# Optimization experiments

Hardware: AMD Instinct MI355X
Metric: run time of the kernel (lower is better)

## Reference

```python
import jax, jax.numpy as jnp
import numpy as np

N_NODES = 10000
N_EDGES = 160000
N_HEADS = 2
N_IN = 16   # fc input dim = x channels (15) + 1 dist channel
N_OUT = 32
ALPHA = 0.2
B, T_LEN = 2, 8


def setup_inputs() -> dict:
    key = jax.random.key(0)
    ks = jax.random.split(key, 6)
    x = jax.random.normal(ks[0], (B, T_LEN, N_NODES, N_IN - 1), dtype=jnp.float32)
    d_ew = jax.random.uniform(ks[1], (N_EDGES + N_NODES, N_HEADS), dtype=jnp.float32)
    u_edges = jax.random.randint(ks[2], (N_EDGES, 2), 0, N_NODES, dtype=jnp.int64)
    u_dist = jax.random.uniform(ks[3], (N_EDGES,), dtype=jnp.float32)
    W = jax.random.normal(ks[4], (N_OUT, N_IN), dtype=jnp.float32) * (1.0 / np.sqrt(N_IN))
    b = jax.random.normal(ks[5], (N_OUT,), dtype=jnp.float32) * 0.01
    return {"x": x, "T": T_LEN, "d_ew": d_ew, "u_edges": u_edges,
            "u_dist": u_dist, "W": W, "b": b}


def reference(x, T, d_ew, u_edges, u_dist, W, b):
    # d_edges = [u_edges; self-loops], d_dist = [u_dist; zeros]
    loops = jnp.arange(N_NODES, dtype=u_edges.dtype)
    d_edges = jnp.concatenate([u_edges, jnp.stack([loops, loops], axis=1)], axis=0)
    d_dist = jnp.concatenate([u_dist, jnp.zeros((N_NODES,), dtype=u_dist.dtype)], axis=0)
    node_i, node_j = d_edges[:, 0], d_edges[:, 1]

    Bx, t, _, C = x.shape
    # graph convolution: out[:, :, j] = sum_e{j(e)=j} d_ew[e] * x[:, :, i(e)]
    xg = x[:, :, node_i, :]                               # (B, t, E, C)
    msgs = xg[..., None, :] * d_ew[None, None, :, :, None]  # (B, t, E, H, C)
    x_conv = jnp.zeros((Bx, t, N_NODES, N_HEADS, C), dtype=x.dtype)
    x_conv = x_conv.at[:, :, node_j].add(msgs)            # (B, t, N, H, C)

    # dist convolution: (N, H)
    dist_conv = jnp.zeros((N_NODES, N_HEADS), dtype=d_ew.dtype)
    dist_conv = dist_conv.at[node_j].add(d_dist[:, None] * d_ew)

    # concat dist channel, broadcast over (B, t)
    dist_b = jnp.broadcast_to(dist_conv[None, None, :, :, None],
                              (Bx, t, N_NODES, N_HEADS, 1))
    x_feature = jnp.concatenate([x_conv, dist_b], axis=-1)  # (B, t, N, H, C+1)

    x_out = jnp.einsum('btnhc,oc->btnho', x_feature, W) + b

    # temporal alpha-blend (RHS uses pre-update values, as in torch slice assign)
    x_out = jnp.concatenate(
        [x_out[:, :1], ALPHA * x_out[:, :-1] + (1.0 - ALPHA) * x_out[:, 1:]], axis=1)
    return jax.nn.sigmoid(x_out)
```

## Files before the change

### kernel.cpp

```cpp
#include <hip/hip_runtime.h>
#include <hip/hip_bf16.h>

#define NN 10000
#define NE 160000
#define NBT 16
#define CIN 15
#define HPAD 128
#define BCAP 64
#define NOUT 32
#define ALPHA_F 0.2f

#define TRANS_BLKS 625
#define EDGE_BLKS  625

__device__ __forceinline__ float bf2f(unsigned short u) {
    return __uint_as_float(((unsigned int)u) << 16);
}
__device__ __forceinline__ unsigned short f2bf(float f) {
    __hip_bfloat16 h = __float2bfloat16(f);
    return *(unsigned short*)&h;
}

__global__ __launch_bounds__(256) void zero_ws(int* __restrict__ p) {
    int i = blockIdx.x * 256 + threadIdx.x;
    if (i < NN) p[i] = 0;
}

__global__ __launch_bounds__(256) void prep(const float* __restrict__ x,
                                            const int* __restrict__ edges,
                                            const float* __restrict__ dist,
                                            const float* __restrict__ dew,
                                            unsigned short* __restrict__ xh,
                                            int* __restrict__ cursor,
                                            int2* __restrict__ epay) {
    __shared__ float tile[NBT][16 * CIN];
    int bid = blockIdx.x;
    int tid = threadIdx.x;
    if (bid < TRANS_BLKS) {
        int n0 = bid * 16;
        if (tid < 16 * CIN) {
#pragma unroll
            for (int bt = 0; bt < NBT; ++bt)
                tile[bt][tid] = x[((size_t)bt * NN + n0) * CIN + tid];
        }
        __syncthreads();
        for (int g = tid; g < 16 * 2 * HPAD; g += 256) {
            int ln = g >> 8;
            int r  = g & 255;
            int half = r >> 7;
            int rr = r & 127;
            float v = 0.f;
            if (rr < 120) {
                int bt = half * 8 + rr / CIN;
                int c  = rr % CIN;
                v = tile[bt][ln * CIN + c];
            }
            xh[(size_t)(n0 + ln) * 256 + r] = f2bf(v);
        }
    } else {
        int e = (bid - TRANS_BLKS) * 256 + tid;
        if (e < NE) {
            int2 ed = ((const int2*)edges)[e];
            float2 w = ((const float2*)dew)[e];
            float d = dist[e];
            int pos = atomicAdd(&cursor[ed.y], 1);
            if (pos < BCAP) {
                unsigned int px = (unsigned int)ed.x | ((unsigned int)f2bf(d) << 16);
                unsigned int py = (unsigned int)f2bf(w.x) | ((unsigned int)f2bf(w.y) << 16);
                epay[ed.y * BCAP + pos] = make_int2((int)px, (int)py);
            }
        }
    }
}

__global__ __launch_bounds__(256) void fused_node(const unsigned short* __restrict__ xh,
                                                  const int* __restrict__ cursor,
                                                  const int2* __restrict__ epay,
                                                  const float* __restrict__ dew,
                                                  const float* __restrict__ W,
                                                  const float* __restrict__ bias,
                                                  float* __restrict__ out) {
    __shared__ float s_xc[4][2][256];
    __shared__ float sWt[16][NOUT];
    __shared__ float sb[NOUT];

    int tid = threadIdx.x;
    for (int i = tid; i < 16 * NOUT; i += 256) {
        int c = i >> 5, o = i & 31;
        sWt[c][o] = W[o * 16 + c];
    }
    if (tid < NOUT) sb[tid] = bias[tid];

    const int unit = tid >> 6;
    const int lane = tid & 63;
    const int n = blockIdx.x * 4 + unit;

    int deg = cursor[n];
    if (deg > BCAP) deg = BCAP;
    const int2* bucket = epay + n * BCAP;

    int2 pay = bucket[lane];

    float dd  = bf2f((unsigned short)((unsigned int)pay.x >> 16));
    float w0l = bf2f((unsigned short)((unsigned int)pay.y & 0xFFFFu));
    float w1l = bf2f((unsigned short)((unsigned int)pay.y >> 16));
    float dc0 = (lane < deg) ? dd * w0l : 0.f;
    float dc1 = (lane < deg) ? dd * w1l : 0.f;
#pragma unroll
    for (int m = 32; m; m >>= 1) {
        dc0 += __shfl_xor(dc0, m, 64);
        dc1 += __shfl_xor(dc1, m, 64);
    }

    const char* xbase = (const char*)xh + 8 * lane;
    float a00 = 0.f, a01 = 0.f, a02 = 0.f, a03 = 0.f;
    float a10 = 0.f, a11 = 0.f, a12 = 0.f, a13 = 0.f;
#pragma unroll 8
    for (int k = 0; k < deg; ++k) {
        int sx = __builtin_amdgcn_readlane(pay.x, k);
        int sw = __builtin_amdgcn_readlane(pay.y, k);
        uint2 u = *(const uint2*)(xbase + (size_t)((sx & 0xFFFF) << 9));
        float x0 = __uint_as_float(u.x << 16);
        float x1 = __uint_as_float(u.x & 0xFFFF0000u);
        float x2 = __uint_as_float(u.y << 16);
        float x3 = __uint_as_float(u.y & 0xFFFF0000u);
        float w0 = __uint_as_float((unsigned int)sw << 16);
        float w1 = __uint_as_float((unsigned int)sw & 0xFFFF0000u);
        a00 += w0 * x0; a01 += w0 * x1; a02 += w0 * x2; a03 += w0 * x3;
        a10 += w1 * x0; a11 += w1 * x1; a12 += w1 * x2; a13 += w1 * x3;
    }
    {
        uint2 u = *(const uint2*)(xbase + ((size_t)n << 9));
        float w0 = dew[2 * (NE + n) + 0];
        float w1 = dew[2 * (NE + n) + 1];
        float x0 = __uint_as_float(u.x << 16);
        float x1 = __uint_as_float(u.x & 0xFFFF0000u);
        float x2 = __uint_as_float(u.y << 16);
        float x3 = __uint_as_float(u.y & 0xFFFF0000u);
        a00 += w0 * x0; a01 += w0 * x1; a02 += w0 * x2; a03 += w0 * x3;
        a10 += w1 * x0; a11 += w1 * x1; a12 += w1 * x2; a13 += w1 * x3;
    }
    *(float4*)&s_xc[unit][0][4 * lane] = make_float4(a00, a01, a02, a03);
    *(float4*)&s_xc[unit][1][4 * lane] = make_float4(a10, a11, a12, a13);
    __syncthreads();

    {
        int o = lane & 31;
        int h = lane >> 5;
        float Wr[16];
#pragma unroll
        for (int c = 0; c < 16; ++c) Wr[c] = sWt[c][o];
        float base = sb[o] + Wr[15] * (h ? dc1 : dc0);
        const float* xc = s_xc[unit][h];
#pragma unroll
        for (int b = 0; b < 2; ++b) {
            float prev = 0.f;
#pragma unroll
            for (int t = 0; t < 8; ++t) {
                const float* xt = xc + b * HPAD + t * CIN;
                float y = base;
#pragma unroll
                for (int c = 0; c < CIN; ++c) y += Wr[c] * xt[c];
                float v = (t == 0) ? y : (ALPHA_F * prev + (1.f - ALPHA_F) * y);
                float sg = 1.f / (1.f + __expf(-v));
                __builtin_nontemporal_store(sg,
                    &out[(((size_t)(b * 8 + t) * NN + n) * 2 + h) * NOUT + o]);
                prev = y;
            }
        }
    }
}

extern "C" void kernel_launch(void* const* d_in, const int* in_sizes, int n_in,
                              void* d_out, int out_size, void* d_ws, size_t ws_size,
                              hipStream_t stream) {
    const float* x     = (const float*)d_in[0];
    const float* dew   = (const float*)d_in[2];
    const int*   edges = (const int*)d_in[3];
    const float* dist  = (const float*)d_in[4];
    const float* W     = (const float*)d_in[5];
    const float* bias  = (const float*)d_in[6];
    float* out = (float*)d_out;

    unsigned short* xh = (unsigned short*)d_ws;
    int2* epay   = (int2*)(xh + (size_t)NN * 256);
    int* cursor  = (int*)(epay + (size_t)NN * BCAP);

    zero_ws<<<(NN + 255) / 256, 256, 0, stream>>>(cursor);
    prep<<<TRANS_BLKS + EDGE_BLKS, 256, 0, stream>>>(x, edges, dist, dew,
                                                     xh, cursor, epay);
    fused_node<<<2500, 256, 0, stream>>>(xh, cursor, epay, dew, W, bias, out);
}
```

Measured before the change: 52.21 us.

## Pad per-timestep features to 16 channels and drop block barrier in node kernel

The bf16 node-feature buffer is re-laid out so each (batch,time) slot holds 16 channels, with channel 15 zeroed. The fused kernel can then read each timestep's conv features from shared memory as four float4 loads instead of 15 scalar loads. W and the bias are loaded straight from global memory into registers rather than staged through shared memory. That removes the block-wide __syncthreads, which becomes a wave-local LDS wait, since each 64-lane unit only reads its own shared slice. The risk is more per-thread global loads of W and a correctness dependence on one unit mapping to exactly one wavefront.

```diff
diff --git a/kernel.cpp b/kernel.cpp
--- a/kernel.cpp
+++ b/kernel.cpp
@@ -44,17 +44,12 @@
                 tile[bt][tid] = x[((size_t)bt * NN + n0) * CIN + tid];
         }
         __syncthreads();
-        for (int g = tid; g < 16 * 2 * HPAD; g += 256) {
+        for (int g = tid; g < 16 * 256; g += 256) {
             int ln = g >> 8;
             int r  = g & 255;
-            int half = r >> 7;
-            int rr = r & 127;
-            float v = 0.f;
-            if (rr < 120) {
-                int bt = half * 8 + rr / CIN;
-                int c  = rr % CIN;
-                v = tile[bt][ln * CIN + c];
-            }
+            int c  = r & 15;
+            int bt = r >> 4;
+            float v = (c < 15) ? tile[bt][ln * CIN + c] : 0.f;
             xh[(size_t)(n0 + ln) * 256 + r] = f2bf(v);
         }
     } else {
@@ -81,25 +76,24 @@
                                                   const float* __restrict__ bias,
                                                   float* __restrict__ out) {
     __shared__ float s_xc[4][2][256];
-    __shared__ float sWt[16][NOUT];
-    __shared__ float sb[NOUT];
 
-    int tid = threadIdx.x;
-    for (int i = tid; i < 16 * NOUT; i += 256) {
-        int c = i >> 5, o = i & 31;
-        sWt[c][o] = W[o * 16 + c];
-    }
-    if (tid < NOUT) sb[tid] = bias[tid];
-
+    const int tid = threadIdx.x;
     const int unit = tid >> 6;
     const int lane = tid & 63;
     const int n = blockIdx.x * 4 + unit;
+    const int o = lane & 31;
+    const int h = lane >> 5;
+
+    float4 w0_ = *(const float4*)(W + o * 16);
+    float4 w1_ = *(const float4*)(W + o * 16 + 4);
+    float4 w2_ = *(const float4*)(W + o * 16 + 8);
+    float4 w3_ = *(const float4*)(W + o * 16 + 12);
+    float bo = bias[o];
 
     int deg = cursor[n];
     if (deg > BCAP) deg = BCAP;
-    const int2* bucket = epay + n * BCAP;
 
-    int2 pay = bucket[lane];
+    int2 pay = epay[n * BCAP + lane];
 
     float dd  = bf2f((unsigned short)((unsigned int)pay.x >> 16));
     float w0l = bf2f((unsigned short)((unsigned int)pay.y & 0xFFFFu));
@@ -142,25 +136,31 @@
     }
     *(float4*)&s_xc[unit][0][4 * lane] = make_float4(a00, a01, a02, a03);
     *(float4*)&s_xc[unit][1][4 * lane] = make_float4(a10, a11, a12, a13);
-    __syncthreads();
+
+    asm volatile("s_waitcnt lgkmcnt(0)" ::: "memory");
 
     {
-        int o = lane & 31;
-        int h = lane >> 5;
-        float Wr[16];
-#pragma unroll
-        for (int c = 0; c < 16; ++c) Wr[c] = sWt[c][o];
-        float base = sb[o] + Wr[15] * (h ? dc1 : dc0);
+        float Wr[16] = { w0_.x, w0_.y, w0_.z, w0_.w,
+                         w1_.x, w1_.y, w1_.z, w1_.w,
+                         w2_.x, w2_.y, w2_.z, w2_.w,
+                         w3_.x, w3_.y, w3_.z, w3_.w };
+        float base = bo + Wr[15] * (h ? dc1 : dc0);
         const float* xc = s_xc[unit][h];
 #pragma unroll
         for (int b = 0; b < 2; ++b) {
             float prev = 0.f;
 #pragma unroll
             for (int t = 0; t < 8; ++t) {
-                const float* xt = xc + b * HPAD + t * CIN;
+                const float* xt = xc + b * HPAD + t * 16;
+                float4 v0 = *(const float4*)(xt);
+                float4 v1 = *(const float4*)(xt + 4);
+                float4 v2 = *(const float4*)(xt + 8);
+                float4 v3 = *(const float4*)(xt + 12);
                 float y = base;
-#pragma unroll
-                for (int c = 0; c < CIN; ++c) y += Wr[c] * xt[c];
+                y += Wr[0]*v0.x + Wr[1]*v0.y + Wr[2]*v0.z + Wr[3]*v0.w;
+                y += Wr[4]*v1.x + Wr[5]*v1.y + Wr[6]*v1.z + Wr[7]*v1.w;
+                y += Wr[8]*v2.x + Wr[9]*v2.y + Wr[10]*v2.z + Wr[11]*v2.w;
+                y += Wr[12]*v3.x + Wr[13]*v3.y + Wr[14]*v3.z + Wr[15]*v3.w;
                 float v = (t == 0) ? y : (ALPHA_F * prev + (1.f - ALPHA_F) * y);
                 float sg = 1.f / (1.f + __expf(-v));
                 __builtin_nontemporal_store(sg,
```

Result: faster. 49.99 us (-4.3%).
